# Performance work log

Measured on AMD Instinct MI355X. Metric: run time of the kernel, lower is better.

Reference implementation:

```python
import jax, jax.numpy as jnp
import numpy as np

# Production-scale dims: b=8, t=1024, emb=1024, heads=16 -> head dim s=64.
B, T, E, H = 8, 1024, 1024, 16
S = E // H  # 64, per-head dim; tokeys/toqueries/tovalues are Linear(S, S) shared across heads


def setup_inputs() -> dict:
    key = jax.random.key(0)
    k0, k1, k2, k3, k4, k5 = jax.random.split(key, 6)
    return {
        "x": jax.random.normal(k0, (B, T, E), dtype=jnp.float32),
        # full lengths: keeps the length-mask path live without all--inf rows (NaN softmax)
        "lengths": jnp.full((B,), T, dtype=jnp.int32),
        # torch Linear stores weight as (out_features, in_features); y = x @ W.T
        "Wk": jax.random.normal(k1, (S, S), dtype=jnp.float32) / np.float32(np.sqrt(S)),
        "Wq": jax.random.normal(k2, (S, S), dtype=jnp.float32) / np.float32(np.sqrt(S)),
        "Wv": jax.random.normal(k3, (S, S), dtype=jnp.float32) / np.float32(np.sqrt(S)),
        "Wu": jax.random.normal(k4, (E, E), dtype=jnp.float32) / np.float32(np.sqrt(E)),
        "bu": jax.random.normal(k5, (E,), dtype=jnp.float32) * jnp.float32(0.02),
    }


def reference(x, lengths, Wk, Wq, Wv, Wu, bu):
    b, t, e = x.shape
    h = H
    s = e // h
    xh = x.reshape(b, t, h, s)

    # per-head projections (same S x S weight for every head), torch Linear: x @ W.T
    queries = jnp.einsum('bths,os->btho', xh, Wq)
    keys = jnp.einsum('bths,os->btho', xh, Wk)
    values = jnp.einsum('bths,os->btho', xh, Wv)

    # scale q and k each by e**-0.25 (net 1/sqrt(e) on scores)
    scale = jnp.float32(e) ** jnp.float32(-0.25)
    dot = jnp.einsum('bqho,bkho->bhqk', queries * scale, keys * scale)  # (b,h,t,t)

    # causal mask (mask_diagonal=False -> strictly upper triangle masked)
    i = jnp.arange(t)[:, None]
    j = jnp.arange(t)[None, :]
    causal = j <= i  # (t,t)
    # length mask over key positions: key index k < lengths[b]
    lenmask = jnp.arange(t)[None, :] < lengths[:, None]  # (b,t)
    valid = causal[None, None, :, :] & lenmask[:, None, None, :]  # (b,1->h,t,t)

    dot = jnp.where(valid, dot, -jnp.inf)
    attn = jax.nn.softmax(dot, axis=-1)

    out = jnp.einsum('bhqk,bkho->bqho', attn, values).reshape(b, t, e)
    return jnp.einsum('bte,oe->bto', out, Wu) + bu
```

## Files before the change

### kernel.cpp

```cpp
#include <hip/hip_runtime.h>
#include <stdint.h>

#define B_ 8
#define T_ 1024
#define E_ 1024
#define H_ 16
#define S_ 64

typedef __attribute__((ext_vector_type(8))) short bf16x8;
typedef __attribute__((ext_vector_type(4))) short bf16x4;
typedef __attribute__((ext_vector_type(4))) float f32x4;

__device__ __forceinline__ f32x4 mfma_pv(bf16x4 a, bf16x4 b, f32x4 c) {
  return __builtin_amdgcn_mfma_f32_16x16x16bf16_1k(a, b, c, 0, 0, 0);
}

__device__ __forceinline__ float e2(float x) { return __builtin_amdgcn_exp2f(x); }

__device__ __forceinline__ ushort f2bf(float f) {
  union { float f; uint32_t u; } v; v.f = f;
  uint32_t r = (v.u + 0x7FFFu + ((v.u >> 16) & 1u)) >> 16;
  return (ushort)r;
}
__device__ __forceinline__ float bf2f(ushort u) {
  union { uint32_t u; float f; } v; v.u = ((uint32_t)u) << 16;
  return v.f;
}

__device__ __forceinline__ uint32_t cvtpk(float a, float b) {
  uint32_t r;
  asm("v_cvt_pk_bf16_f32 %0, %1, %2" : "=v"(r) : "v"(a), "v"(b));
  return r;
}
__device__ __forceinline__ bf16x4 pack4(const float* p) {
  union { uint32_t u[2]; bf16x4 v; } pu;
  pu.u[0] = cvtpk(p[0], p[1]);
  pu.u[1] = cvtpk(p[2], p[3]);
  return pu.v;
}

__device__ __forceinline__ void gload_lds16(const ushort* g, ushort* l) {
  __builtin_amdgcn_global_load_lds(
      (const __attribute__((address_space(1))) uint32_t*)g,
      (__attribute__((address_space(3))) uint32_t*)l, 16, 0, 0);
}

__device__ __forceinline__ bf16x8 load8(const void* p, size_t idx, bool isf32) {
  if (isf32) {
    const float* fp = (const float*)p + idx;
    f32x4 f0 = *(const f32x4*)(fp);
    f32x4 f1 = *(const f32x4*)(fp + 4);
    union { uint32_t u[4]; bf16x8 v; } r;
    r.u[0] = cvtpk(f0[0], f0[1]);
    r.u[1] = cvtpk(f0[2], f0[3]);
    r.u[2] = cvtpk(f1[0], f1[1]);
    r.u[3] = cvtpk(f1[2], f1[3]);
    return r.v;
  }
  return *(const bf16x8*)((const ushort*)p + idx);
}

__device__ __forceinline__ bool detect_f32_wave(const uint32_t* __restrict__ x) {
  const int lane = threadIdx.x & 63;
  int sane = 0;
  #pragma unroll
  for (int j = 0; j < 4; ++j) {
    uint32_t lo = x[lane * 4 + j] & 0xFFFFu;
    uint32_t e = (lo >> 7) & 0xFFu;
    sane += (e >= 96u && e <= 158u) ? 1 : 0;
  }
  #pragma unroll
  for (int off = 32; off >= 1; off >>= 1) sane += __shfl_xor(sane, off);
  return sane < 192;
}

__global__ __launch_bounds__(256) void cvt_kernel(
    const void* __restrict__ x,
    const void* __restrict__ Wu, const void* __restrict__ bu,
    const void* __restrict__ Wq, const void* __restrict__ Wk,
    const void* __restrict__ Wv,
    ushort* __restrict__ wub, ushort* __restrict__ bub,
    ushort* __restrict__ wqkv) {
  const bool f32 = detect_f32_wave((const uint32_t*)x);
  if (blockIdx.x < 512) {
    size_t base = (size_t)blockIdx.x * 2048 + threadIdx.x * 8;
    *(bf16x8*)(wub + base) = load8(Wu, base, f32);
  } else if (blockIdx.x == 512) {
    if (threadIdx.x < 128) {
      size_t base = (size_t)threadIdx.x * 8;
      *(bf16x8*)(bub + base) = load8(bu, base, f32);
    }
  } else {
    const void* Ws[3] = {Wq, Wk, Wv};
    int idx = blockIdx.x - 513;
    int w = idx >> 1, half = idx & 1;
    size_t base = (size_t)half * 2048 + threadIdx.x * 8;
    *(bf16x8*)(wqkv + w * 4096 + base) = load8(Ws[w], base, f32);
  }
}

#define QSCALE 0.045084220f

__global__ __launch_bounds__(256) void qkv_kernel(
    const void* __restrict__ x, const ushort* __restrict__ wqkv,
    ushort* __restrict__ qb, ushort* __restrict__ kb, ushort* __restrict__ vb) {
  __shared__ ushort qs[64 * 72];
  __shared__ ushort ks[64 * 72];
  __shared__ ushort vs[64 * 72];
  const bool f32 = detect_f32_wave((const uint32_t*)x);
  const int tid = threadIdx.x;
  const int lane = tid & 63, wave = tid >> 6;
  const int m = lane & 15, quad = lane >> 4;
  const int tile = blockIdx.x & 15;
  const int h = (blockIdx.x >> 4) & 15;
  const int b = blockIdx.x >> 8;
  const int t0 = tile * 64;

  const size_t xrow = ((size_t)b * T_ + t0 + wave * 16 + m) * E_ + h * S_;
  bf16x8 a0 = load8(x, xrow + quad * 8, f32);
  bf16x8 a1 = load8(x, xrow + 32 + quad * 8, f32);

  #pragma unroll
  for (int w = 0; w < 3; ++w) {
    const float sc = (w == 0) ? QSCALE : 1.0f;
    ushort* dst = (w == 0) ? qs : (w == 1) ? ks : vs;
    #pragma unroll
    for (int nt = 0; nt < 4; ++nt) {
      const ushort* wrow = wqkv + w * 4096 + (nt * 16 + m) * S_;
      bf16x8 b0 = *(const bf16x8*)(wrow + quad * 8);
      bf16x8 b1 = *(const bf16x8*)(wrow + 32 + quad * 8);
      f32x4 acc = {0.f, 0.f, 0.f, 0.f};
      acc = __builtin_amdgcn_mfma_f32_16x16x32_bf16(a0, b0, acc, 0, 0, 0);
      acc = __builtin_amdgcn_mfma_f32_16x16x32_bf16(a1, b1, acc, 0, 0, 0);
      #pragma unroll
      for (int i = 0; i < 4; ++i) {
        int lr = wave * 16 + quad * 4 + i;
        int o  = nt * 16 + m;
        if (w == 2) {
          vs[o * 72 + lr] = f2bf(acc[i]);
        } else {
          dst[lr * 72 + o] = f2bf(acc[i] * sc);
        }
      }
    }
  }

  __syncthreads();

  const int row = tid >> 2, ck = (tid & 3) * 16;
  const size_t qkbase = (((size_t)b * H_ + h) * T_ + t0 + row) * S_ + ck;
  *(bf16x8*)(qb + qkbase)     = *(const bf16x8*)(qs + row * 72 + ck);
  *(bf16x8*)(qb + qkbase + 8) = *(const bf16x8*)(qs + row * 72 + ck + 8);
  *(bf16x8*)(kb + qkbase)     = *(const bf16x8*)(ks + row * 72 + ck);
  *(bf16x8*)(kb + qkbase + 8) = *(const bf16x8*)(ks + row * 72 + ck + 8);
  const size_t vbase = (((size_t)b * H_ + h) * S_ + row) * T_ + t0 + ck;
  *(bf16x8*)(vb + vbase)      = *(const bf16x8*)(vs + row * 72 + ck);
  *(bf16x8*)(vb + vbase + 8)  = *(const bf16x8*)(vs + row * 72 + ck + 8);
}

__global__ __launch_bounds__(256, 3) void attn_kernel(
    const ushort* __restrict__ qb, const ushort* __restrict__ kb,
    const ushort* __restrict__ vb, const int* __restrict__ lengths,
    ushort* __restrict__ ao) {
  __shared__ ushort klds[2][64 * 64];
  __shared__ ushort vlds[2][64 * 64];

  const int tid = threadIdx.x;
  const int lane = tid & 63, wave = tid >> 6;
  const int m = lane & 15, quad = lane >> 4;
  const int ord = blockIdx.x >> 7;
  const int bh = blockIdx.x & 127;
  const int b  = bh >> 4, h = bh & 15;
  const int qt = 15 - ord;
  const int len = lengths[b];

  const size_t head_off = ((size_t)b * H_ + h) * (size_t)T_ * S_;
  const ushort* Q  = qb + head_off;
  const ushort* K  = kb + head_off;
  const ushort* Vt = vb + head_off;

  const int sr  = lane >> 3;
  const int ssw = 8 * ((lane & 7) ^ sr);
  const int swzr = 8 * (m & 7);

  const int qw = qt * 64 + wave * 16;
  bf16x8 aq0 = *(const bf16x8*)(Q + (size_t)(qw + m) * S_ + quad * 8);
  bf16x8 aq1 = *(const bf16x8*)(Q + (size_t)(qw + m) * S_ + 32 + quad * 8);

  const int qmin = min(qw + m, len - 1);

  f32x4 o[4], Lacc;
  #pragma unroll
  for (int i = 0; i < 4; ++i) o[i] = (f32x4){0.f, 0.f, 0.f, 0.f};
  Lacc = (f32x4){0.f, 0.f, 0.f, 0.f};

  bf16x4 ones;
  #pragma unroll
  for (int i = 0; i < 4; ++i) ones[i] = (short)0x3F80;

  #pragma unroll
  for (int p = 0; p < 2; ++p) {
    const int wrow = wave * 16 + p * 8;
    gload_lds16(K  + (size_t)(wrow + sr) * S_ + ssw, &klds[0][wrow * 64]);
    gload_lds16(Vt + (size_t)(wrow + sr) * T_ + ssw, &vlds[0][wrow * 64]);
  }
  __syncthreads();

  for (int kt = 0; kt <= qt; ++kt) {
    const bool msk = (kt == qt) || ((kt + 1) * 64 > len);

    if (kt < qt) {
      const ushort* Kn = K + (size_t)(kt + 1) * 64 * S_;
      #pragma unroll
      for (int p = 0; p < 2; ++p) {
        const int wrow = wave * 16 + p * 8;
        gload_lds16(Kn + (size_t)(wrow + sr) * S_ + ssw,
                    &klds[(kt + 1) & 1][wrow * 64]);
        gload_lds16(Vt + (size_t)(wrow + sr) * T_ + (kt + 1) * 64 + ssw,
                    &vlds[(kt + 1) & 1][wrow * 64]);
      }
    }

    const ushort* kls = klds[kt & 1];
    const ushort* vls = vlds[kt & 1];

    bf16x4 vv[4][4];
    #pragma unroll
    for (int nt = 0; nt < 4; ++nt) {
      #pragma unroll
      for (int v4 = 0; v4 < 4; ++v4) {
        vv[nt][v4] = *(const bf16x4*)(vls + (v4 * 16 + m) * 64 +
                                      8 * ((2 * nt + (quad >> 1)) ^ (m & 7)) +
                                      (quad & 1) * 4);
      }
    }

    bf16x4 pf[4];
    #pragma unroll
    for (int nt = 0; nt < 4; ++nt) {
      const ushort* krow = kls + (nt * 16 + m) * 64;
      bf16x8 ak0 = *(const bf16x8*)(krow + ((8 * quad) ^ swzr));
      bf16x8 ak1 = *(const bf16x8*)(krow + ((32 + 8 * quad) ^ swzr));
      const int kl0 = kt * 64 + nt * 16 + quad * 4;

      __builtin_amdgcn_s_setprio(1);
      f32x4 s4 = {0.f, 0.f, 0.f, 0.f};
      s4 = __builtin_amdgcn_mfma_f32_16x16x32_bf16(ak0, aq0, s4, 0, 0, 0);
      s4 = __builtin_amdgcn_mfma_f32_16x16x32_bf16(ak1, aq1, s4, 0, 0, 0);
      __builtin_amdgcn_s_setprio(0);

      float p4[4];
      #pragma unroll
      for (int i = 0; i < 4; ++i) {
        float s = s4[i];
        if (msk) s = (kl0 + i <= qmin) ? s : -1e30f;
        p4[i] = e2(s);
      }
      pf[nt] = pack4(p4);
    }

    __builtin_amdgcn_s_setprio(1);
    #pragma unroll
    for (int nt = 0; nt < 4; ++nt) {
      Lacc = mfma_pv(pf[nt], ones, Lacc);
      #pragma unroll
      for (int v4 = 0; v4 < 4; ++v4)
        o[v4] = mfma_pv(pf[nt], vv[nt][v4], o[v4]);
    }
    __builtin_amdgcn_s_setprio(0);

    if (kt < qt) __syncthreads();
  }

  #pragma unroll
  for (int i = 0; i < 4; ++i) {
    float il = (Lacc[i] > 0.f) ? 1.0f / Lacc[i] : 0.f;
    size_t base = ((size_t)b * T_ + qw + quad * 4 + i) * E_ + h * 64;
    #pragma unroll
    for (int v4 = 0; v4 < 4; ++v4)
      ao[base + v4 * 16 + m] = f2bf(o[v4][i] * il);
  }
}

__global__ __launch_bounds__(256) void proj_kernel(
    const ushort* __restrict__ A, const ushort* __restrict__ Wu,
    const ushort* __restrict__ bu, float* __restrict__ Y) {
  __shared__ ushort As[128 * 72];
  __shared__ ushort Bs[128 * 72];
  const int tid = threadIdx.x;
  const int lane = tid & 63, wave = tid >> 6;
  const int m = lane & 15, quad = lane >> 4;
  const int m0 = blockIdx.x * 128, n0 = blockIdx.y * 128;
  const int wm = (wave & 1) * 64, wn = (wave >> 1) * 64;

  f32x4 acc[4][4];
  #pragma unroll
  for (int i = 0; i < 4; ++i)
    #pragma unroll
    for (int j = 0; j < 4; ++j) acc[i][j] = (f32x4){0.f, 0.f, 0.f, 0.f};

  bf16x8 pa[4], pb[4];
  #pragma unroll
  for (int p = 0; p < 4; ++p) {
    int c = tid + p * 256;
    int row = c >> 3, col = (c & 7) * 8;
    pa[p] = *(const bf16x8*)(A + (size_t)(m0 + row) * E_ + col);
    pb[p] = *(const bf16x8*)(Wu + (size_t)(n0 + row) * E_ + col);
  }

  for (int k0 = 0; k0 < E_; k0 += 64) {
    __syncthreads();
    #pragma unroll
    for (int p = 0; p < 4; ++p) {
      int c = tid + p * 256;
      int row = c >> 3, col = (c & 7) * 8;
      *(bf16x8*)(As + row * 72 + col) = pa[p];
      *(bf16x8*)(Bs + row * 72 + col) = pb[p];
    }
    __syncthreads();

    if (k0 + 64 < E_) {
      #pragma unroll
      for (int p = 0; p < 4; ++p) {
        int c = tid + p * 256;
        int row = c >> 3, col = (c & 7) * 8;
        pa[p] = *(const bf16x8*)(A + (size_t)(m0 + row) * E_ + k0 + 64 + col);
        pb[p] = *(const bf16x8*)(Wu + (size_t)(n0 + row) * E_ + k0 + 64 + col);
      }
    }

    #pragma unroll
    for (int kk = 0; kk < 64; kk += 32) {
      bf16x8 af[4], bfrag[4];
      #pragma unroll
      for (int i = 0; i < 4; ++i)
        af[i] = *(const bf16x8*)(As + (wm + i * 16 + m) * 72 + kk + quad * 8);
      #pragma unroll
      for (int j = 0; j < 4; ++j)
        bfrag[j] = *(const bf16x8*)(Bs + (wn + j * 16 + m) * 72 + kk + quad * 8);
      #pragma unroll
      for (int i = 0; i < 4; ++i)
        #pragma unroll
        for (int j = 0; j < 4; ++j)
          acc[i][j] = __builtin_amdgcn_mfma_f32_16x16x32_bf16(af[i], bfrag[j], acc[i][j], 0, 0, 0);
    }
  }

  #pragma unroll
  for (int j = 0; j < 4; ++j) {
    float bias = bf2f(bu[n0 + wn + j * 16 + m]);
    #pragma unroll
    for (int i = 0; i < 4; ++i) {
      #pragma unroll
      for (int r = 0; r < 4; ++r) {
        int grow = m0 + wm + i * 16 + quad * 4 + r;
        int gcol = n0 + wn + j * 16 + m;
        Y[(size_t)grow * E_ + gcol] = acc[i][j][r] + bias;
      }
    }
  }
}

extern "C" void kernel_launch(void* const* d_in, const int* in_sizes, int n_in,
                              void* d_out, int out_size, void* d_ws, size_t ws_size,
                              hipStream_t stream) {
  const void* x  = d_in[0];
  const int* lengths = (const int*)d_in[1];
  const void* Wk = d_in[2];
  const void* Wq = d_in[3];
  const void* Wv = d_in[4];
  const void* Wu = d_in[5];
  const void* bu = d_in[6];
  float* out = (float*)d_out;

  const size_t hsz = (size_t)B_ * H_ * T_ * S_;
  ushort* qb   = (ushort*)d_ws;
  ushort* kb   = qb + hsz;
  ushort* vb   = kb + hsz;
  ushort* ao   = vb + hsz;
  ushort* wub  = ao + hsz;
  ushort* bub  = wub + (size_t)E_ * E_;
  ushort* wqkv = bub + E_;

  cvt_kernel<<<dim3(519), dim3(256), 0, stream>>>(x, Wu, bu, Wq, Wk, Wv, wub, bub, wqkv);
  qkv_kernel<<<dim3(B_ * H_ * (T_ / 64)), dim3(256), 0, stream>>>(x, wqkv, qb, kb, vb);
  attn_kernel<<<dim3(B_ * H_ * 16), dim3(256), 0, stream>>>(qb, kb, vb, lengths, ao);
  proj_kernel<<<dim3((B_ * T_) / 128, E_ / 128), dim3(256), 0, stream>>>(ao, wub, bub, out);
}
```

Baseline: 183.4 us.

## Load V fragments directly from global into registers, double-buffered across steps

```diff
diff --git a/kernel.cpp b/kernel.cpp
--- a/kernel.cpp
+++ b/kernel.cpp
@@ -158,12 +158,67 @@
   *(bf16x8*)(vb + vbase + 8)  = *(const bf16x8*)(vs + row * 72 + ck + 8);
 }
 
-__global__ __launch_bounds__(256, 3) void attn_kernel(
+#define VLOAD(DST, KT)                                                        \
+  _Pragma("unroll")                                                           \
+  for (int v4 = 0; v4 < 4; ++v4) {                                            \
+    _Pragma("unroll")                                                         \
+    for (int nt = 0; nt < 4; ++nt) {                                          \
+      DST[nt][v4] = *(const bf16x4*)(vbase + (size_t)(v4 * 16) * T_ +         \
+                                     (KT) * 64 + nt * 16);                    \
+    }                                                                         \
+  }
+
+#define ATTN_STEP(KT, VCUR, VNEXT, KREAD, KWRITE)                             \
+  {                                                                           \
+    const int kt_ = (KT);                                                     \
+    const bool msk_ = (kt_ == qt) || ((kt_ + 1) * 64 > len);                  \
+    if (kt_ < qt) {                                                           \
+      const ushort* Kn_ = K + (size_t)(kt_ + 1) * 64 * S_;                    \
+      _Pragma("unroll")                                                       \
+      for (int p = 0; p < 2; ++p) {                                           \
+        const int wrow = wave * 16 + p * 8;                                   \
+        gload_lds16(Kn_ + (size_t)(wrow + sr) * S_ + ssw, (KWRITE) + wrow * 64); \
+      }                                                                       \
+      VLOAD(VNEXT, kt_ + 1)                                                   \
+    }                                                                         \
+    bf16x4 pf[4];                                                             \
+    _Pragma("unroll")                                                         \
+    for (int nt = 0; nt < 4; ++nt) {                                          \
+      const ushort* krow = (KREAD) + (nt * 16 + m) * 64;                      \
+      bf16x8 ak0 = *(const bf16x8*)(krow + ((8 * quad) ^ swzr));              \
+      bf16x8 ak1 = *(const bf16x8*)(krow + ((32 + 8 * quad) ^ swzr));         \
+      const int kl0 = kt_ * 64 + nt * 16 + quad * 4;                          \
+      __builtin_amdgcn_s_setprio(1);                                          \
+      f32x4 s4 = {0.f, 0.f, 0.f, 0.f};                                        \
+      s4 = __builtin_amdgcn_mfma_f32_16x16x32_bf16(ak0, aq0, s4, 0, 0, 0);    \
+      s4 = __builtin_amdgcn_mfma_f32_16x16x32_bf16(ak1, aq1, s4, 0, 0, 0);    \
+      __builtin_amdgcn_s_setprio(0);                                          \
+      float p4[4];                                                            \
+      _Pragma("unroll")                                                       \
+      for (int i = 0; i < 4; ++i) {                                           \
+        float s = s4[i];                                                      \
+        if (msk_) s = (kl0 + i <= qmin) ? s : -1e30f;                         \
+        p4[i] = e2(s);                                                        \
+      }                                                                       \
+      pf[nt] = pack4(p4);                                                     \
+    }                                                                         \
+    __builtin_amdgcn_s_setprio(1);                                            \
+    _Pragma("unroll")                                                         \
+    for (int nt = 0; nt < 4; ++nt) {                                          \
+      Lacc = mfma_pv(pf[nt], ones, Lacc);                                     \
+      _Pragma("unroll")                                                       \
+      for (int v4 = 0; v4 < 4; ++v4)                                          \
+        o[v4] = mfma_pv(pf[nt], VCUR[nt][v4], o[v4]);                         \
+    }                                                                         \
+    __builtin_amdgcn_s_setprio(0);                                            \
+    if (kt_ < qt) __syncthreads();                                            \
+  }
+
+__global__ __launch_bounds__(256) void attn_kernel(
     const ushort* __restrict__ qb, const ushort* __restrict__ kb,
     const ushort* __restrict__ vb, const int* __restrict__ lengths,
     ushort* __restrict__ ao) {
   __shared__ ushort klds[2][64 * 64];
-  __shared__ ushort vlds[2][64 * 64];
 
   const int tid = threadIdx.x;
   const int lane = tid & 63, wave = tid >> 6;
@@ -189,6 +244,8 @@
 
   const int qmin = min(qw + m, len - 1);
 
+  const ushort* vbase = Vt + (size_t)m * T_ + quad * 4;
+
   f32x4 o[4], Lacc;
   #pragma unroll
   for (int i = 0; i < 4; ++i) o[i] = (f32x4){0.f, 0.f, 0.f, 0.f};
@@ -198,78 +255,21 @@
   #pragma unroll
   for (int i = 0; i < 4; ++i) ones[i] = (short)0x3F80;
 
+  bf16x4 vvA[4][4], vvB[4][4];
+
   #pragma unroll
   for (int p = 0; p < 2; ++p) {
     const int wrow = wave * 16 + p * 8;
-    gload_lds16(K  + (size_t)(wrow + sr) * S_ + ssw, &klds[0][wrow * 64]);
-    gload_lds16(Vt + (size_t)(wrow + sr) * T_ + ssw, &vlds[0][wrow * 64]);
-  }
+    gload_lds16(K + (size_t)(wrow + sr) * S_ + ssw, &klds[0][wrow * 64]);
+  }
+  VLOAD(vvA, 0)
   __syncthreads();
 
-  for (int kt = 0; kt <= qt; ++kt) {
-    const bool msk = (kt == qt) || ((kt + 1) * 64 > len);
-
-    if (kt < qt) {
-      const ushort* Kn = K + (size_t)(kt + 1) * 64 * S_;
-      #pragma unroll
-      for (int p = 0; p < 2; ++p) {
-        const int wrow = wave * 16 + p * 8;
-        gload_lds16(Kn + (size_t)(wrow + sr) * S_ + ssw,
-                    &klds[(kt + 1) & 1][wrow * 64]);
-        gload_lds16(Vt + (size_t)(wrow + sr) * T_ + (kt + 1) * 64 + ssw,
-                    &vlds[(kt + 1) & 1][wrow * 64]);
-      }
-    }
-
-    const ushort* kls = klds[kt & 1];
-    const ushort* vls = vlds[kt & 1];
-
-    bf16x4 vv[4][4];
-    #pragma unroll
-    for (int nt = 0; nt < 4; ++nt) {
-      #pragma unroll
-      for (int v4 = 0; v4 < 4; ++v4) {
-        vv[nt][v4] = *(const bf16x4*)(vls + (v4 * 16 + m) * 64 +
-                                      8 * ((2 * nt + (quad >> 1)) ^ (m & 7)) +
-                                      (quad & 1) * 4);
-      }
-    }
-
-    bf16x4 pf[4];
-    #pragma unroll
-    for (int nt = 0; nt < 4; ++nt) {
-      const ushort* krow = kls + (nt * 16 + m) * 64;
-      bf16x8 ak0 = *(const bf16x8*)(krow + ((8 * quad) ^ swzr));
-      bf16x8 ak1 = *(const bf16x8*)(krow + ((32 + 8 * quad) ^ swzr));
-      const int kl0 = kt * 64 + nt * 16 + quad * 4;
-
-      __builtin_amdgcn_s_setprio(1);
-      f32x4 s4 = {0.f, 0.f, 0.f, 0.f};
-      s4 = __builtin_amdgcn_mfma_f32_16x16x32_bf16(ak0, aq0, s4, 0, 0, 0);
-      s4 = __builtin_amdgcn_mfma_f32_16x16x32_bf16(ak1, aq1, s4, 0, 0, 0);
-      __builtin_amdgcn_s_setprio(0);
-
-      float p4[4];
-      #pragma unroll
-      for (int i = 0; i < 4; ++i) {
-        float s = s4[i];
-        if (msk) s = (kl0 + i <= qmin) ? s : -1e30f;
-        p4[i] = e2(s);
-      }
-      pf[nt] = pack4(p4);
-    }
-
-    __builtin_amdgcn_s_setprio(1);
-    #pragma unroll
-    for (int nt = 0; nt < 4; ++nt) {
-      Lacc = mfma_pv(pf[nt], ones, Lacc);
-      #pragma unroll
-      for (int v4 = 0; v4 < 4; ++v4)
-        o[v4] = mfma_pv(pf[nt], vv[nt][v4], o[v4]);
-    }
-    __builtin_amdgcn_s_setprio(0);
-
-    if (kt < qt) __syncthreads();
+  for (int kt = 0; kt <= qt; kt += 2) {
+    ATTN_STEP(kt, vvA, vvB, klds[0], klds[1])
+    if (kt + 1 <= qt) {
+      ATTN_STEP(kt + 1, vvB, vvA, klds[1], klds[0])
+    }
   }
 
   #pragma unroll
```

New measurement: 277.5 us. +51.3%, slower.
